# Optimization experiments

Measured on AMD Instinct MI355X. Metric: run time of the kernel, lower is better.

The kernel has to match this reference:

```python
import jax, jax.numpy as jnp
import numpy as np

OUTPUT_SIZE = 512
MEMORY_SIZE = 64
N_HALF = 131072          # terrain / population vision length each
N_EDGES = 16777216       # enabled connections
NUM_INPUT_NODES = 2 * N_HALF + MEMORY_SIZE * OUTPUT_SIZE + 1  # +1 bias


def setup_inputs() -> dict:
    key = jax.random.key(0)
    k = jax.random.split(key, 5)
    return {
        "terrain": jax.random.normal(k[0], (N_HALF,), dtype=jnp.float32),
        "population": jax.random.normal(k[1], (N_HALF,), dtype=jnp.float32),
        "memory": jnp.zeros((MEMORY_SIZE, OUTPUT_SIZE), dtype=jnp.float32),
        "src": jax.random.randint(k[2], (N_EDGES,), 0, NUM_INPUT_NODES),
        "dst": jax.random.randint(k[3], (N_EDGES,), 0, OUTPUT_SIZE),
        "w": jax.random.normal(k[4], (N_EDGES,), dtype=jnp.float32),
    }


def reference(terrain, population, memory, src, dst, w):
    # Build the flat input-node activation vector exactly like forward():
    # [terrain, population, memory.flatten(), bias=1]
    x = jnp.concatenate([
        terrain,
        population,
        memory.reshape(-1),
        jnp.ones((1,), dtype=terrain.dtype),
    ])  # [NUM_INPUT_NODES]
    # Per-edge weighted gather, then scatter-add into output nodes.
    # Output nodes use identity activation (only hidden nodes get ReLU,
    # and the minimal-init topology has input->output edges only).
    contrib = x[src] * w                                   # [N_EDGES]
    out = jax.ops.segment_sum(contrib, dst, num_segments=OUTPUT_SIZE)
    return out[None, :]  # [1, OUTPUT_SIZE], matching torch.stack(..., dim=1)
```

## Files before the change

### kernel.cpp

```cpp
#include <hip/hip_runtime.h>

#define N_HALF   131072
#define MEM_ELEMS (64 * 512)
#define NIN      (2 * N_HALF + MEM_ELEMS + 1)
#define NEDGES   16777216
#define NOUT     512
#define TPB      256

#define NGROUPS       (NEDGES / 4)
#define HALF_GROUPS   (NGROUPS / 2)
#define GPB           2048
#define NBLK_HALF     (HALF_GROUPS / GPB)
#define NROWS         (2 * NBLK_HALF)

#define RBLK          128
#define ROWS_PER_BLK  (NROWS / RBLK)

typedef int   vint4   __attribute__((ext_vector_type(4)));
typedef float vfloat4 __attribute__((ext_vector_type(4)));

__global__ __launch_bounds__(TPB) void build_x_kernel(
    const float* __restrict__ terrain,
    const float* __restrict__ pop,
    const float* __restrict__ mem,
    float* __restrict__ x,
    float* __restrict__ out)
{
    int i = blockIdx.x * TPB + threadIdx.x;
    if (i < NOUT) out[i] = 0.0f;
    if (i >= NIN) return;
    float v;
    if (i < N_HALF)            v = terrain[i];
    else if (i < 2 * N_HALF)   v = pop[i - N_HALF];
    else if (i < NIN - 1)      v = mem[i - 2 * N_HALF];
    else                       v = 1.0f;
    x[i] = v;
}

__device__ __forceinline__ float fetch_direct(int s,
    const float* __restrict__ terrain,
    const float* __restrict__ pop,
    const float* __restrict__ mem)
{
    if (s < 2 * N_HALF)
        return (s < N_HALF) ? terrain[s] : pop[s - N_HALF];
    return (s < NIN - 1) ? mem[s - 2 * N_HALF] : 1.0f;
}

__global__ __launch_bounds__(TPB) void zero_out_kernel(float* __restrict__ out)
{
    int i = blockIdx.x * TPB + threadIdx.x;
    if (i < NOUT) out[i] = 0.0f;
}

template <int G, int REPS>
__global__ __launch_bounds__(TPB) void edge_deep_kernel(
    const vint4*   __restrict__ src4,
    const vint4*   __restrict__ dst4,
    const vfloat4* __restrict__ w4,
    const float*   __restrict__ x,
    float* __restrict__ partials,
    int groupBase, int rowBase)
{
    __shared__ float acc[NOUT];
    const int t = threadIdx.x;
    acc[t] = 0.0f;
    acc[t + TPB] = 0.0f;
    __syncthreads();

    const int base = groupBase + blockIdx.x * GPB + t;

#pragma unroll
    for (int rep = 0; rep < REPS; ++rep) {
        const int rb = base + rep * (G * TPB);

        vint4   s[G];
        vint4   d[G];
        vfloat4 wv[G];
#pragma unroll
        for (int u = 0; u < G; ++u)
            s[u] = __builtin_nontemporal_load(&src4[rb + u * TPB]);
#pragma unroll
        for (int u = 0; u < G; ++u)
            d[u] = __builtin_nontemporal_load(&dst4[rb + u * TPB]);
#pragma unroll
        for (int u = 0; u < G; ++u)
            wv[u] = __builtin_nontemporal_load(&w4[rb + u * TPB]);

        float g[G][4];
#pragma unroll
        for (int u = 0; u < G; ++u) {
            g[u][0] = x[s[u].x];
            g[u][1] = x[s[u].y];
            g[u][2] = x[s[u].z];
            g[u][3] = x[s[u].w];
        }

#pragma unroll
        for (int u = 0; u < G; ++u) {
            unsafeAtomicAdd(&acc[d[u].x], g[u][0] * wv[u].x);
            unsafeAtomicAdd(&acc[d[u].y], g[u][1] * wv[u].y);
            unsafeAtomicAdd(&acc[d[u].z], g[u][2] * wv[u].z);
            unsafeAtomicAdd(&acc[d[u].w], g[u][3] * wv[u].w);
        }
    }
    __syncthreads();

    const size_t row = (size_t)(rowBase + blockIdx.x) * NOUT;
    partials[row + t]       = acc[t];
    partials[row + t + TPB] = acc[t + TPB];
}

template <int MODE>
__global__ __launch_bounds__(TPB) void edge_fallback_kernel(
    const vint4*   __restrict__ src4,
    const vint4*   __restrict__ dst4,
    const vfloat4* __restrict__ w4,
    const float*   __restrict__ x,
    const float*   __restrict__ terrain,
    const float*   __restrict__ pop,
    const float*   __restrict__ mem,
    float* __restrict__ outp)
{
    __shared__ float acc[NOUT];
    const int t = threadIdx.x;
    acc[t] = 0.0f;
    acc[t + TPB] = 0.0f;
    __syncthreads();

    const int base = blockIdx.x * GPB + t;
    for (int j = 0; j < GPB / TPB; ++j) {
        const int gi = base + j * TPB;
        vint4   s = src4[gi];
        vint4   d = dst4[gi];
        vfloat4 w = w4[gi];
        float g0, g1, g2, g3;
        if (MODE == 2) {
            g0 = fetch_direct(s.x, terrain, pop, mem);
            g1 = fetch_direct(s.y, terrain, pop, mem);
            g2 = fetch_direct(s.z, terrain, pop, mem);
            g3 = fetch_direct(s.w, terrain, pop, mem);
        } else {
            g0 = x[s.x]; g1 = x[s.y]; g2 = x[s.z]; g3 = x[s.w];
        }
        unsafeAtomicAdd(&acc[d.x], g0 * w.x);
        unsafeAtomicAdd(&acc[d.y], g1 * w.y);
        unsafeAtomicAdd(&acc[d.z], g2 * w.z);
        unsafeAtomicAdd(&acc[d.w], g3 * w.w);
    }
    __syncthreads();
    unsafeAtomicAdd(&outp[t],       acc[t]);
    unsafeAtomicAdd(&outp[t + TPB], acc[t + TPB]);
}

__global__ __launch_bounds__(128) void reduce_kernel(
    const float* __restrict__ partials, float* __restrict__ out)
{
    const vfloat4* __restrict__ p4 = (const vfloat4*)partials;
    const int t  = threadIdx.x;
    const int r0 = blockIdx.x * ROWS_PER_BLK;
    vfloat4 s = {0.f, 0.f, 0.f, 0.f};
#pragma unroll
    for (int r = 0; r < ROWS_PER_BLK; ++r) {
        vfloat4 v = p4[(size_t)(r0 + r) * (NOUT / 4) + t];
        s += v;
    }
    unsafeAtomicAdd(&out[t * 4 + 0], s.x);
    unsafeAtomicAdd(&out[t * 4 + 1], s.y);
    unsafeAtomicAdd(&out[t * 4 + 2], s.z);
    unsafeAtomicAdd(&out[t * 4 + 3], s.w);
}

extern "C" void kernel_launch(void* const* d_in, const int* in_sizes, int n_in,
                              void* d_out, int out_size, void* d_ws, size_t ws_size,
                              hipStream_t stream)
{
    const float* terrain = (const float*)d_in[0];
    const float* pop     = (const float*)d_in[1];
    const float* mem     = (const float*)d_in[2];
    const int*   src     = (const int*)d_in[3];
    const int*   dst     = (const int*)d_in[4];
    const float* w       = (const float*)d_in[5];
    float* out = (float*)d_out;

    const size_t X_BYTES  = (size_t)NIN * 4;
    const size_t PART_OFF = 1179904;
    const size_t NEED     = PART_OFF + (size_t)NROWS * NOUT * 4;

    float* x        = (float*)d_ws;
    float* partials = (float*)((char*)d_ws + PART_OFF);

    if (ws_size >= NEED) {
        build_x_kernel<<<(NIN + TPB - 1) / TPB, TPB, 0, stream>>>(terrain, pop, mem, x, out);
        edge_deep_kernel<4, 2><<<NBLK_HALF, TPB, 0, stream>>>(
            (const vint4*)src, (const vint4*)dst, (const vfloat4*)w,
            x, partials, 0, 0);
        edge_deep_kernel<8, 1><<<NBLK_HALF, TPB, 0, stream>>>(
            (const vint4*)src, (const vint4*)dst, (const vfloat4*)w,
            x, partials, HALF_GROUPS, NBLK_HALF);
        reduce_kernel<<<RBLK, 128, 0, stream>>>(partials, out);
    } else if (ws_size >= X_BYTES) {
        build_x_kernel<<<(NIN + TPB - 1) / TPB, TPB, 0, stream>>>(terrain, pop, mem, x, out);
        edge_fallback_kernel<1><<<NGROUPS / GPB, TPB, 0, stream>>>(
            (const vint4*)src, (const vint4*)dst, (const vfloat4*)w,
            x, terrain, pop, mem, out);
    } else {
        zero_out_kernel<<<(NOUT + TPB - 1) / TPB, TPB, 0, stream>>>(out);
        edge_fallback_kernel<2><<<NGROUPS / GPB, TPB, 0, stream>>>(
            (const vint4*)src, (const vint4*)dst, (const vfloat4*)w,
            nullptr, terrain, pop, mem, out);
    }
}
```

Measured before the change: 280.2 us.

## Privatize LDS histograms per wave and atomically reduce into 32 partial rows

Merges the two edge kernels into one launch with four times as many smaller blocks. Each wavefront now accumulates into its own 512-bin LDS histogram, which cuts shared-memory atomic contention. At block end the four copies are summed and added with global atomics into one of 32 workspace rows, replacing the per-block partial rows and the large reduction. The cost is far more global atomic traffic (every block flushes 512 atomics), extra per-block setup and flush work from halving work per block, and a build kernel that now also zeroes the accumulator rows.

```diff
diff --git a/kernel.cpp b/kernel.cpp
--- a/kernel.cpp
+++ b/kernel.cpp
@@ -7,14 +7,12 @@
 #define NOUT     512
 #define TPB      256
 
-#define NGROUPS       (NEDGES / 4)
-#define HALF_GROUPS   (NGROUPS / 2)
-#define GPB           2048
-#define NBLK_HALF     (HALF_GROUPS / GPB)
-#define NROWS         (2 * NBLK_HALF)
-
-#define RBLK          128
-#define ROWS_PER_BLK  (NROWS / RBLK)
+#define NGROUPS   (NEDGES / 4)
+#define G         4
+#define GPB       (TPB * G)
+#define NBLK_E    (NGROUPS / GPB)
+#define NACC      32
+#define ACC_FLOATS (NACC * NOUT)
 
 typedef int   vint4   __attribute__((ext_vector_type(4)));
 typedef float vfloat4 __attribute__((ext_vector_type(4)));
@@ -24,10 +22,10 @@
     const float* __restrict__ pop,
     const float* __restrict__ mem,
     float* __restrict__ x,
-    float* __restrict__ out)
+    float* __restrict__ partials)
 {
     int i = blockIdx.x * TPB + threadIdx.x;
-    if (i < NOUT) out[i] = 0.0f;
+    if (i < ACC_FLOATS) partials[i] = 0.0f;
     if (i >= NIN) return;
     float v;
     if (i < N_HALF)            v = terrain[i];
@@ -53,62 +51,61 @@
     if (i < NOUT) out[i] = 0.0f;
 }
 
-template <int G, int REPS>
-__global__ __launch_bounds__(TPB) void edge_deep_kernel(
+__global__ __launch_bounds__(TPB) void edge_kernel(
     const vint4*   __restrict__ src4,
     const vint4*   __restrict__ dst4,
     const vfloat4* __restrict__ w4,
     const float*   __restrict__ x,
-    float* __restrict__ partials,
-    int groupBase, int rowBase)
-{
-    __shared__ float acc[NOUT];
-    const int t = threadIdx.x;
-    acc[t] = 0.0f;
-    acc[t + TPB] = 0.0f;
-    __syncthreads();
-
-    const int base = groupBase + blockIdx.x * GPB + t;
-
-#pragma unroll
-    for (int rep = 0; rep < REPS; ++rep) {
-        const int rb = base + rep * (G * TPB);
-
-        vint4   s[G];
-        vint4   d[G];
-        vfloat4 wv[G];
-#pragma unroll
-        for (int u = 0; u < G; ++u)
-            s[u] = __builtin_nontemporal_load(&src4[rb + u * TPB]);
-#pragma unroll
-        for (int u = 0; u < G; ++u)
-            d[u] = __builtin_nontemporal_load(&dst4[rb + u * TPB]);
-#pragma unroll
-        for (int u = 0; u < G; ++u)
-            wv[u] = __builtin_nontemporal_load(&w4[rb + u * TPB]);
-
-        float g[G][4];
-#pragma unroll
-        for (int u = 0; u < G; ++u) {
-            g[u][0] = x[s[u].x];
-            g[u][1] = x[s[u].y];
-            g[u][2] = x[s[u].z];
-            g[u][3] = x[s[u].w];
-        }
-
-#pragma unroll
-        for (int u = 0; u < G; ++u) {
-            unsafeAtomicAdd(&acc[d[u].x], g[u][0] * wv[u].x);
-            unsafeAtomicAdd(&acc[d[u].y], g[u][1] * wv[u].y);
-            unsafeAtomicAdd(&acc[d[u].z], g[u][2] * wv[u].z);
-            unsafeAtomicAdd(&acc[d[u].w], g[u][3] * wv[u].w);
-        }
-    }
-    __syncthreads();
-
-    const size_t row = (size_t)(rowBase + blockIdx.x) * NOUT;
-    partials[row + t]       = acc[t];
-    partials[row + t + TPB] = acc[t + TPB];
+    float* __restrict__ partials)
+{
+    __shared__ float acc[4][NOUT];
+    const int t   = threadIdx.x;
+    const int wid = t >> 6;
+#pragma unroll
+    for (int k = 0; k < 8; ++k)
+        acc[(t * 8 + k) >> 9][(t * 8 + k) & (NOUT - 1)] = 0.0f;
+    __syncthreads();
+
+    const int base = blockIdx.x * GPB + t;
+
+    vint4   s[G];
+    vint4   d[G];
+    vfloat4 wv[G];
+#pragma unroll
+    for (int u = 0; u < G; ++u)
+        s[u] = __builtin_nontemporal_load(&src4[base + u * TPB]);
+#pragma unroll
+    for (int u = 0; u < G; ++u)
+        d[u] = __builtin_nontemporal_load(&dst4[base + u * TPB]);
+#pragma unroll
+    for (int u = 0; u < G; ++u)
+        wv[u] = __builtin_nontemporal_load(&w4[base + u * TPB]);
+
+    float g[G][4];
+#pragma unroll
+    for (int u = 0; u < G; ++u) {
+        g[u][0] = x[s[u].x];
+        g[u][1] = x[s[u].y];
+        g[u][2] = x[s[u].z];
+        g[u][3] = x[s[u].w];
+    }
+
+#pragma unroll
+    for (int u = 0; u < G; ++u) {
+        unsafeAtomicAdd(&acc[wid][d[u].x], g[u][0] * wv[u].x);
+        unsafeAtomicAdd(&acc[wid][d[u].y], g[u][1] * wv[u].y);
+        unsafeAtomicAdd(&acc[wid][d[u].z], g[u][2] * wv[u].z);
+        unsafeAtomicAdd(&acc[wid][d[u].w], g[u][3] * wv[u].w);
+    }
+    __syncthreads();
+
+    float* prow = partials + (size_t)(blockIdx.x & (NACC - 1)) * NOUT;
+#pragma unroll
+    for (int k = 0; k < 2; ++k) {
+        const int slot = t + k * TPB;
+        const float v = acc[0][slot] + acc[1][slot] + acc[2][slot] + acc[3][slot];
+        unsafeAtomicAdd(&prow[slot], v);
+    }
 }
 
 template <int MODE>
@@ -129,7 +126,7 @@
     __syncthreads();
 
     const int base = blockIdx.x * GPB + t;
-    for (int j = 0; j < GPB / TPB; ++j) {
+    for (int j = 0; j < G; ++j) {
         const int gi = base + j * TPB;
         vint4   s = src4[gi];
         vint4   d = dst4[gi];
@@ -153,22 +150,15 @@
     unsafeAtomicAdd(&outp[t + TPB], acc[t + TPB]);
 }
 
-__global__ __launch_bounds__(128) void reduce_kernel(
+__global__ __launch_bounds__(TPB) void reduce_kernel(
     const float* __restrict__ partials, float* __restrict__ out)
 {
-    const vfloat4* __restrict__ p4 = (const vfloat4*)partials;
-    const int t  = threadIdx.x;
-    const int r0 = blockIdx.x * ROWS_PER_BLK;
-    vfloat4 s = {0.f, 0.f, 0.f, 0.f};
-#pragma unroll
-    for (int r = 0; r < ROWS_PER_BLK; ++r) {
-        vfloat4 v = p4[(size_t)(r0 + r) * (NOUT / 4) + t];
-        s += v;
-    }
-    unsafeAtomicAdd(&out[t * 4 + 0], s.x);
-    unsafeAtomicAdd(&out[t * 4 + 1], s.y);
-    unsafeAtomicAdd(&out[t * 4 + 2], s.z);
-    unsafeAtomicAdd(&out[t * 4 + 3], s.w);
+    const int c = blockIdx.x * TPB + threadIdx.x;
+    float s = 0.0f;
+#pragma unroll
+    for (int r = 0; r < NACC; ++r)
+        s += partials[(size_t)r * NOUT + c];
+    out[c] = s;
 }
 
 extern "C" void kernel_launch(void* const* d_in, const int* in_sizes, int n_in,
@@ -185,28 +175,27 @@
 
     const size_t X_BYTES  = (size_t)NIN * 4;
     const size_t PART_OFF = 1179904;
-    const size_t NEED     = PART_OFF + (size_t)NROWS * NOUT * 4;
+    const size_t NEED     = PART_OFF + (size_t)ACC_FLOATS * 4;
 
     float* x        = (float*)d_ws;
     float* partials = (float*)((char*)d_ws + PART_OFF);
 
     if (ws_size >= NEED) {
-        build_x_kernel<<<(NIN + TPB - 1) / TPB, TPB, 0, stream>>>(terrain, pop, mem, x, out);
-        edge_deep_kernel<4, 2><<<NBLK_HALF, TPB, 0, stream>>>(
-            (const vint4*)src, (const vint4*)dst, (const vfloat4*)w,
-            x, partials, 0, 0);
-        edge_deep_kernel<8, 1><<<NBLK_HALF, TPB, 0, stream>>>(
-            (const vint4*)src, (const vint4*)dst, (const vfloat4*)w,
-            x, partials, HALF_GROUPS, NBLK_HALF);
-        reduce_kernel<<<RBLK, 128, 0, stream>>>(partials, out);
+        build_x_kernel<<<(NIN + TPB - 1) / TPB, TPB, 0, stream>>>(
+            terrain, pop, mem, x, partials);
+        edge_kernel<<<NBLK_E, TPB, 0, stream>>>(
+            (const vint4*)src, (const vint4*)dst, (const vfloat4*)w, x, partials);
+        reduce_kernel<<<NOUT / TPB, TPB, 0, stream>>>(partials, out);
     } else if (ws_size >= X_BYTES) {
-        build_x_kernel<<<(NIN + TPB - 1) / TPB, TPB, 0, stream>>>(terrain, pop, mem, x, out);
-        edge_fallback_kernel<1><<<NGROUPS / GPB, TPB, 0, stream>>>(
+        build_x_kernel<<<(NIN + TPB - 1) / TPB, TPB, 0, stream>>>(
+            terrain, pop, mem, x, (float*)d_ws);
+        zero_out_kernel<<<2, TPB, 0, stream>>>(out);
+        edge_fallback_kernel<1><<<NBLK_E, TPB, 0, stream>>>(
             (const vint4*)src, (const vint4*)dst, (const vfloat4*)w,
             x, terrain, pop, mem, out);
     } else {
-        zero_out_kernel<<<(NOUT + TPB - 1) / TPB, TPB, 0, stream>>>(out);
-        edge_fallback_kernel<2><<<NGROUPS / GPB, TPB, 0, stream>>>(
+        zero_out_kernel<<<2, TPB, 0, stream>>>(out);
+        edge_fallback_kernel<2><<<NBLK_E, TPB, 0, stream>>>(
             (const vint4*)src, (const vint4*)dst, (const vfloat4*)w,
             nullptr, terrain, pop, mem, out);
     }
```

Result: faster. 262.1 us (-6.5%).
